# Kernel optimization log

Hardware: AMD Instinct MI355X
Metric: run time of the kernel (lower is better)

## Reference

```python
import jax, jax.numpy as jnp
import numpy as np

DIM = 1024
HEADS = 16
HEAD_DIM = DIM // HEADS  # 64
EPS = 1e-5


def layer_norm(x, w, b):
    # LayerNorm over last dim (head_dim), matching nn.LayerNorm defaults
    mu = jnp.mean(x, axis=-1, keepdims=True)
    var = jnp.mean(jnp.square(x - mu), axis=-1, keepdims=True)
    return (x - mu) * jax.lax.rsqrt(var + EPS) * w + b


def apply_rotary_emb(x, freqs):
    # x: [B, S, H, D]; freqs: [S, D/2] angles. Interleaved (complex) rotary:
    # pairs (x[2i], x[2i+1]) rotated by angle freqs[:, i].
    x1 = x[..., 0::2]
    x2 = x[..., 1::2]
    cos = jnp.cos(freqs)[None, :, None, :]
    sin = jnp.sin(freqs)[None, :, None, :]
    r1 = x1 * cos - x2 * sin
    r2 = x1 * sin + x2 * cos
    return jnp.stack([r1, r2], axis=-1).reshape(x.shape)


def setup_inputs() -> dict:
    key = jax.random.key(0)
    ks = jax.random.split(key, 8)
    B, S = 2, 2048
    x = jax.random.normal(ks[0], (B, S, DIM), dtype=jnp.float32)
    freqs = jax.random.uniform(ks[1], (S, HEAD_DIM // 2), dtype=jnp.float32)
    sc = 1.0 / np.sqrt(DIM)
    w_qkv = jax.random.normal(ks[2], (DIM, 4 * DIM), dtype=jnp.float32) * sc
    w_out = jax.random.normal(ks[3], (DIM, DIM), dtype=jnp.float32) * sc
    qn_w = jnp.ones((HEAD_DIM,), jnp.float32)
    qn_b = jnp.zeros((HEAD_DIM,), jnp.float32)
    kn_w = jnp.ones((HEAD_DIM,), jnp.float32)
    kn_b = jnp.zeros((HEAD_DIM,), jnp.float32)
    return {"x": x, "freqs": freqs, "w_qkv": w_qkv, "w_out": w_out,
            "qn_w": qn_w, "qn_b": qn_b, "kn_w": kn_w, "kn_b": kn_b}


def reference(x, freqs, w_qkv, w_out, qn_w, qn_b, kn_w, kn_b):
    B, S, _ = x.shape
    qkv = x @ w_qkv  # [B, S, 4*DIM]
    q, k, v, gate = jnp.split(qkv, 4, axis=-1)
    q = q.reshape(B, S, HEADS, HEAD_DIM)
    k = k.reshape(B, S, HEADS, HEAD_DIM)
    v = v.reshape(B, S, HEADS, HEAD_DIM)
    q = layer_norm(q, qn_w, qn_b)
    k = layer_norm(k, kn_w, kn_b)
    q = apply_rotary_emb(q, freqs)
    k = apply_rotary_emb(k, freqs)
    # flash_attn_func: non-causal softmax attention, scale 1/sqrt(head_dim)
    scale = 1.0 / np.sqrt(HEAD_DIM)
    scores = jnp.einsum('bqhd,bkhd->bhqk', q, k) * scale
    probs = jax.nn.softmax(scores, axis=-1)
    o = jnp.einsum('bhqk,bkhd->bqhd', probs, v)
    o = o.reshape(B, S, DIM)
    o = o * jax.nn.sigmoid(gate)
    return o @ w_out
```

## Files before the change

kernel.cpp:

```cpp
#include <hip/hip_runtime.h>


typedef _Float16 f16;
typedef _Float16 f16x8 __attribute__((ext_vector_type(8)));
typedef _Float16 f16x4 __attribute__((ext_vector_type(4)));
typedef float    f32x4 __attribute__((ext_vector_type(4)));

#define MFMA16(a, b, c) __builtin_amdgcn_mfma_f32_16x16x32_f16((a), (b), (c), 0, 0, 0)

__device__ __forceinline__ void gload16(const void* g, void* l) {
  __builtin_amdgcn_global_load_lds(
      (const __attribute__((address_space(1))) void*)g,
      (__attribute__((address_space(3))) void*)l, 16, 0, 0);
}

__device__ __forceinline__ float exp2_fast(float x) {
#if __has_builtin(__builtin_amdgcn_exp2f)
  return __builtin_amdgcn_exp2f(x);
#else
  float r;
  asm("v_exp_f32 %0, %1" : "=v"(r) : "v"(x));
  return r;
#endif
}
__device__ __forceinline__ unsigned pkrtz(float a, float b) {
  typedef __fp16 hf16x2 __attribute__((ext_vector_type(2)));
  union { hf16x2 h; unsigned u; } c;
  c.h = __builtin_amdgcn_cvt_pkrtz(a, b);
  return c.u;
}

__global__ void rope_table_kernel(const float* __restrict__ freqs, float* __restrict__ tbl) {
  int i = blockIdx.x * 256 + threadIdx.x;
  if (i >= 2048 * 32) return;
  int s = i >> 5, j = i & 31;
  float f = freqs[i];
  tbl[s * 64 + j]      = cosf(f);
  tbl[s * 64 + 32 + j] = sinf(f);
}

__global__ void cast_f16_kernel(const float* __restrict__ in, f16* __restrict__ out, int n8) {
  int i = blockIdx.x * 256 + threadIdx.x;
  if (i >= n8) return;
  float4 a = ((const float4*)in)[2 * i];
  float4 b = ((const float4*)in)[2 * i + 1];
  f16x8 o;
  o[0] = (f16)a.x; o[1] = (f16)a.y; o[2] = (f16)a.z; o[3] = (f16)a.w;
  o[4] = (f16)b.x; o[5] = (f16)b.y; o[6] = (f16)b.z; o[7] = (f16)b.w;
  ((f16x8*)out)[i] = o;
}

__global__ void transpose_cast_kernel(const float* __restrict__ in, f16* __restrict__ out,
                                      int R, int C) {
  __shared__ float t[64][65];
  int c0 = blockIdx.x * 64, r0 = blockIdx.y * 64;
  int tx = threadIdx.x & 15, ty = threadIdx.x >> 4;
#pragma unroll
  for (int i = 0; i < 4; ++i) {
    float4 v = *(const float4*)&in[(size_t)(r0 + ty + 16 * i) * C + c0 + tx * 4];
    t[ty + 16 * i][tx * 4 + 0] = v.x;
    t[ty + 16 * i][tx * 4 + 1] = v.y;
    t[ty + 16 * i][tx * 4 + 2] = v.z;
    t[ty + 16 * i][tx * 4 + 3] = v.w;
  }
  __syncthreads();
#pragma unroll
  for (int i = 0; i < 4; ++i) {
    int n = c0 + ty + 16 * i;
    int k = r0 + tx * 4;
    f16x4 o;
    o[0] = (f16)t[tx * 4 + 0][ty + 16 * i];
    o[1] = (f16)t[tx * 4 + 1][ty + 16 * i];
    o[2] = (f16)t[tx * 4 + 2][ty + 16 * i];
    o[3] = (f16)t[tx * 4 + 3][ty + 16 * i];
    *(f16x4*)&out[(size_t)n * R + k] = o;
  }
}

__global__ void fill_debug_kernel(float* out, int n) {
  int i = blockIdx.x * 256 + threadIdx.x;
  if (i < n) out[i] = 12345.0f;
}

template <int EPI>
__global__ __launch_bounds__(256, 2) void gemm_f16(
    const f16* __restrict__ A, const f16* __restrict__ B,
    float* __restrict__ Cout, int M, int N, int K,
    f16* __restrict__ qraw, f16* __restrict__ kraw,
    f16* __restrict__ g16, f16* __restrict__ v_t) {
  __shared__ f16 sA[2][128 * 64], sB[2][128 * 64];
  const int tid = threadIdx.x, lane = tid & 63;
  const int wave = tid >> 6, wm = wave >> 1, wn = wave & 1;
  const int lg = lane >> 4, lr = lane & 15;
  const int n0 = blockIdx.x * 128, m0 = blockIdx.y * 128;

  auto stg = [&](int k0, int p) {
#pragma unroll
    for (int r = 0; r < 4; ++r) {
      int off = (tid + r * 256) * 16;
      int row = off >> 7;
      int col = ((off & 127) ^ ((row & 7) << 4)) >> 1;
      gload16(A + (size_t)(m0 + row) * K + k0 + col, (char*)sA[p] + off);
      gload16(B + (size_t)(n0 + row) * K + k0 + col, (char*)sB[p] + off);
    }
  };

  f32x4 acc[4][4];
#pragma unroll
  for (int m = 0; m < 4; ++m)
#pragma unroll
    for (int n = 0; n < 4; ++n) acc[m][n] = (f32x4){0.f, 0.f, 0.f, 0.f};

  stg(0, 0);
  const int NT = K >> 6;
  int cur = 0;
  for (int t = 0; t < NT; ++t, cur ^= 1) {
    __syncthreads();
    if (t + 1 < NT) stg((t + 1) << 6, cur ^ 1);
#pragma unroll
    for (int ks = 0; ks < 2; ++ks) {
      f16x8 bfr[4];
#pragma unroll
      for (int n = 0; n < 4; ++n) {
        int row = wn * 64 + n * 16 + lr;
        int boff = (row << 7) + (ks << 6) + (lg << 4);
        boff ^= (row & 7) << 4;
        bfr[n] = *(const f16x8*)((const char*)sB[cur] + boff);
      }
#pragma unroll
      for (int m = 0; m < 4; ++m) {
        int row = wm * 64 + m * 16 + lr;
        int aoff = (row << 7) + (ks << 6) + (lg << 4);
        aoff ^= (row & 7) << 4;
        f16x8 afr = *(const f16x8*)((const char*)sA[cur] + aoff);
#pragma unroll
        for (int n = 0; n < 4; ++n) acc[m][n] = MFMA16(afr, bfr[n], acc[m][n]);
      }
    }
  }

  if (EPI == 0) {
#pragma unroll
    for (int m = 0; m < 4; ++m) {
      int row = m0 + wm * 64 + m * 16 + 4 * lg;
#pragma unroll
      for (int n = 0; n < 4; ++n) {
        int col = n0 + wn * 64 + n * 16 + lr;
#pragma unroll
        for (int r = 0; r < 4; ++r) Cout[(size_t)(row + r) * N + col] = acc[m][n][r];
      }
    }
  } else {
    const int region = n0 >> 10;
    if (region == 2) {
#pragma unroll
      for (int m = 0; m < 4; ++m) {
        int row = m0 + wm * 64 + m * 16 + 4 * lg;
#pragma unroll
        for (int n = 0; n < 4; ++n) {
          int col = n0 + wn * 64 + n * 16 + lr;
          int c = col - 2048, hh = c >> 6, d = c & 63;
          int bb = row >> 11, s = row & 2047;
          f16x4 pv;
          pv[0] = (f16)acc[m][n][0];
          pv[1] = (f16)acc[m][n][1];
          pv[2] = (f16)acc[m][n][2];
          pv[3] = (f16)acc[m][n][3];
          *(f16x4*)&v_t[(size_t)((bb * 16 + hh) * 64 + d) * 2048 + s] = pv;
        }
      }
    } else if (region == 3) {
#pragma unroll
      for (int m = 0; m < 4; ++m) {
        int row = m0 + wm * 64 + m * 16 + 4 * lg;
#pragma unroll
        for (int n = 0; n < 4; ++n) {
          int col = (n0 & 1023) + wn * 64 + n * 16 + lr;
#pragma unroll
          for (int r = 0; r < 4; ++r) {
            float sg = 1.0f / (1.0f + exp2_fast(acc[m][n][r] * -1.44269504f));
            g16[(size_t)(row + r) * 1024 + col] = (f16)sg;
          }
        }
      }
    } else {
      f16* dst = region ? kraw : qraw;
#pragma unroll
      for (int m = 0; m < 4; ++m) {
        int row = m0 + wm * 64 + m * 16 + 4 * lg;
#pragma unroll
        for (int n = 0; n < 4; ++n) {
          int col = (n0 & 1023) + wn * 64 + n * 16 + lr;
#pragma unroll
          for (int r = 0; r < 4; ++r)
            dst[(size_t)(row + r) * 1024 + col] = (f16)acc[m][n][r];
        }
      }
    }
  }
}

__global__ void norm_rope16_kernel(const f16* __restrict__ qr, const f16* __restrict__ kr,
                                   const float* __restrict__ tbl,
                                   const float* __restrict__ qn_w, const float* __restrict__ qn_b,
                                   const float* __restrict__ kn_w, const float* __restrict__ kn_b,
                                   f16* __restrict__ q_h, f16* __restrict__ k_h) {
  int row = blockIdx.x;
  int s = row & 2047;
  int hh = threadIdx.x >> 4, sub = threadIdx.x & 15;
  int base = row * 1024 + hh * 64 + sub * 4;
  float c0 = tbl[s * 64 + sub * 2 + 0], c1 = tbl[s * 64 + sub * 2 + 1];
  float s0 = tbl[s * 64 + 32 + sub * 2 + 0], s1 = tbl[s * 64 + 32 + sub * 2 + 1];
#pragma unroll
  for (int which = 0; which < 2; ++which) {
    const f16* src = which ? kr : qr;
    const float* wp = which ? kn_w : qn_w;
    const float* bp = which ? kn_b : qn_b;
    f16* dst = which ? k_h : q_h;
    f16x4 xr = *(const f16x4*)&src[base];
    float x0 = (float)xr[0], x1 = (float)xr[1], x2 = (float)xr[2], x3 = (float)xr[3];
    float sum = x0 + x1 + x2 + x3;
    sum += __shfl_xor(sum, 1); sum += __shfl_xor(sum, 2);
    sum += __shfl_xor(sum, 4); sum += __shfl_xor(sum, 8);
    float mu = sum * (1.0f / 64.0f);
    float d0 = x0 - mu, d1 = x1 - mu, d2 = x2 - mu, d3 = x3 - mu;
    float sq = d0 * d0 + d1 * d1 + d2 * d2 + d3 * d3;
    sq += __shfl_xor(sq, 1); sq += __shfl_xor(sq, 2);
    sq += __shfl_xor(sq, 4); sq += __shfl_xor(sq, 8);
    float rstd = rsqrtf(sq * (1.0f / 64.0f) + 1e-5f);
    float4 w = *(const float4*)&wp[sub * 4];
    float4 bb = *(const float4*)&bp[sub * 4];
    float n0 = d0 * rstd * w.x + bb.x;
    float n1 = d1 * rstd * w.y + bb.y;
    float n2 = d2 * rstd * w.z + bb.z;
    float n3 = d3 * rstd * w.w + bb.w;
    float r0 = n0 * c0 - n1 * s0, r1 = n0 * s0 + n1 * c0;
    float r2 = n2 * c1 - n3 * s1, r3 = n2 * s1 + n3 * c1;
    f16x4 ov;
    ov[0] = (f16)r0; ov[1] = (f16)r1; ov[2] = (f16)r2; ov[3] = (f16)r3;
    *(f16x4*)&dst[base] = ov;
  }
}

__global__ __launch_bounds__(256, 2) void attn_kernel(const f16* __restrict__ q_h,
                                                      const f16* __restrict__ k_h,
                                                      const f16* __restrict__ v_t,
                                                      const f16* __restrict__ g16,
                                                      f16* __restrict__ a16) {
  __shared__ __align__(16) char smem[65536];
  const int tid = threadIdx.x, lane = tid & 63, wave = tid >> 6;
  const int lg = lane >> 4, lr = lane & 15;
  const int bh = blockIdx.x >> 4, qt = blockIdx.x & 15;
  const int b = bh >> 4, h = bh & 15;
  const int qrow0 = b * 2048 + qt * 128 + wave * 32;

  auto stage = [&](int kv0, int p) {
    char* kb = smem + p * 16384;
    char* vb = smem + 32768 + p * 16384;
#pragma unroll
    for (int r = 0; r < 4; ++r) {
      int off = (tid + r * 256) * 16;
      {
        int row = off >> 7;
        int col = ((off & 127) ^ ((row & 7) << 4)) >> 1;
        int g = ((row >> 5) << 5) + (((row >> 2) & 3) << 3) + (((row >> 4) & 1) << 2) + (row & 3);
        gload16(&k_h[(size_t)(b * 2048 + kv0 + g) * 1024 + h * 64 + col], kb + off);
      }
      {
        int d = off >> 8;
        int col = ((off & 255) ^ ((d & 15) << 4)) >> 1;
        gload16(&v_t[(size_t)(bh * 64 + d) * 2048 + kv0 + col], vb + off);
      }
    }
  };

  f16x8 qf[2][2];
#pragma unroll
  for (int n = 0; n < 2; ++n)
#pragma unroll
    for (int ks = 0; ks < 2; ++ks)
      qf[n][ks] = *(const f16x8*)&q_h[(size_t)(qrow0 + n * 16 + lr) * 1024 + h * 64 + ks * 32 + lg * 8];

  f16x8 ones;
#pragma unroll
  for (int j = 0; j < 8; ++j) ones[j] = (f16)1.0f;

  f32x4 accO[4][2];
#pragma unroll
  for (int m = 0; m < 4; ++m) {
    accO[m][0] = (f32x4){0.f, 0.f, 0.f, 0.f};
    accO[m][1] = (f32x4){0.f, 0.f, 0.f, 0.f};
  }
  f32x4 accL[2] = {(f32x4){0.f, 0.f, 0.f, 0.f}, (f32x4){0.f, 0.f, 0.f, 0.f}};
  float mrun[2] = {-1e30f, -1e30f};
  const float SCL2 = 0.125f * 1.44269504f;
  const float THRP = 44.36f;
  const f32x4 fz = (f32x4){0.f, 0.f, 0.f, 0.f};

  stage(0, 0);

  int cur = 0;
  for (int t = 0; t < 16; ++t, cur ^= 1) {
    __syncthreads();
    if (t < 15) stage((t + 1) * 128, cur ^ 1);

    const char* kb = smem + cur * 16384;
    const char* vb = smem + 32768 + cur * 16384;

    f32x4 st[8][2];
    __builtin_amdgcn_s_setprio(1);
#pragma unroll
    for (int m = 0; m < 8; ++m) {
      int row = m * 16 + lr;
      int koff0 = ((row << 7) + (lg << 4)) ^ ((row & 7) << 4);
      int koff1 = ((row << 7) + 64 + (lg << 4)) ^ ((row & 7) << 4);
      f16x8 a0 = *(const f16x8*)(kb + koff0);
      f16x8 a1 = *(const f16x8*)(kb + koff1);
      st[m][0] = MFMA16(a1, qf[0][1], MFMA16(a0, qf[0][0], fz));
      st[m][1] = MFMA16(a1, qf[1][1], MFMA16(a0, qf[1][0], fz));
    }
    __builtin_amdgcn_s_setprio(0);

    uint2 pdw[2][8];
#pragma unroll
    for (int n = 0; n < 2; ++n) {
      float t03 = fmaxf(fmaxf(fmaxf(st[0][n][0], st[0][n][1]), fmaxf(st[0][n][2], st[0][n][3])),
                        fmaxf(fmaxf(st[1][n][0], st[1][n][1]), fmaxf(st[1][n][2], st[1][n][3])));
      float t47 = fmaxf(fmaxf(fmaxf(st[2][n][0], st[2][n][1]), fmaxf(st[2][n][2], st[2][n][3])),
                        fmaxf(fmaxf(st[3][n][0], st[3][n][1]), fmaxf(st[3][n][2], st[3][n][3])));
      float t8b = fmaxf(fmaxf(fmaxf(st[4][n][0], st[4][n][1]), fmaxf(st[4][n][2], st[4][n][3])),
                        fmaxf(fmaxf(st[5][n][0], st[5][n][1]), fmaxf(st[5][n][2], st[5][n][3])));
      float tcf = fmaxf(fmaxf(fmaxf(st[6][n][0], st[6][n][1]), fmaxf(st[6][n][2], st[6][n][3])),
                        fmaxf(fmaxf(st[7][n][0], st[7][n][1]), fmaxf(st[7][n][2], st[7][n][3])));
      float vm = fmaxf(fmaxf(t03, t47), fmaxf(t8b, tcf));
      vm = fmaxf(vm, __shfl_xor(vm, 16));
      vm = fmaxf(vm, __shfl_xor(vm, 32));
      if (__any(vm > mrun[n] + THRP)) {
        float mnew = fmaxf(mrun[n], vm);
        float fac = exp2_fast((mrun[n] - mnew) * SCL2);
        mrun[n] = mnew;
        accL[n] *= fac;
#pragma unroll
        for (int m = 0; m < 4; ++m) accO[m][n] *= fac;
      }
      float mc = mrun[n] * SCL2;
#pragma unroll
      for (int m = 0; m < 8; ++m) {
        float p0 = exp2_fast(st[m][n][0] * SCL2 - mc);
        float p1 = exp2_fast(st[m][n][1] * SCL2 - mc);
        float p2 = exp2_fast(st[m][n][2] * SCL2 - mc);
        float p3 = exp2_fast(st[m][n][3] * SCL2 - mc);
        pdw[n][m].x = pkrtz(p0, p1);
        pdw[n][m].y = pkrtz(p2, p3);
      }
    }

    f16x8 pb[2][4];
#pragma unroll
    for (int n = 0; n < 2; ++n)
#pragma unroll
      for (int ks = 0; ks < 4; ++ks) {
        union { uint4 u; f16x8 h; } c;
        c.u = make_uint4(pdw[n][2 * ks].x, pdw[n][2 * ks].y,
                         pdw[n][2 * ks + 1].x, pdw[n][2 * ks + 1].y);
        pb[n][ks] = c.h;
      }
    __builtin_amdgcn_s_setprio(1);
#pragma unroll
    for (int m = 0; m < 4; ++m)
#pragma unroll
      for (int ks = 0; ks < 4; ++ks) {
        int d = m * 16 + lr;
        int voff = (d << 8) + (ks << 6) + (lg << 4);
        voff ^= (d & 15) << 4;
        f16x8 av = *(const f16x8*)(vb + voff);
        accO[m][0] = MFMA16(av, pb[0][ks], accO[m][0]);
        accO[m][1] = MFMA16(av, pb[1][ks], accO[m][1]);
      }
#pragma unroll
    for (int ks = 0; ks < 4; ++ks) {
      accL[0] = MFMA16(ones, pb[0][ks], accL[0]);
      accL[1] = MFMA16(ones, pb[1][ks], accL[1]);
    }
    __builtin_amdgcn_s_setprio(0);
  }

#pragma unroll
  for (int n = 0; n < 2; ++n) {
    float rl = 1.0f / accL[n][0];
    int orow = qrow0 + n * 16 + lr;
#pragma unroll
    for (int m = 0; m < 4; ++m) {
      size_t idx = (size_t)orow * 1024 + h * 64 + m * 16 + lg * 4;
      f16x4 gv = *(const f16x4*)&g16[idx];
      f16x4 ov;
      ov[0] = (f16)(accO[m][n][0] * rl * (float)gv[0]);
      ov[1] = (f16)(accO[m][n][1] * rl * (float)gv[1]);
      ov[2] = (f16)(accO[m][n][2] * rl * (float)gv[2]);
      ov[3] = (f16)(accO[m][n][3] * rl * (float)gv[3]);
      *(f16x4*)&a16[idx] = ov;
    }
  }
}

extern "C" void kernel_launch(void* const* d_in, const int* in_sizes, int n_in,
                              void* d_out, int out_size, void* d_ws, size_t ws_size,
                              hipStream_t stream) {
  const float* x      = (const float*)d_in[0];
  const float* freqs  = (const float*)d_in[1];
  const float* w_qkv  = (const float*)d_in[2];
  const float* w_out  = (const float*)d_in[3];
  const float* qn_w   = (const float*)d_in[4];
  const float* qn_b   = (const float*)d_in[5];
  const float* kn_w   = (const float*)d_in[6];
  const float* kn_b   = (const float*)d_in[7];
  float* out = (float*)d_out;
  char* ws = (char*)d_ws;
  const size_t MB = 1024 * 1024;
  f16*   v_t   = (f16*)(ws + 0);
  f16*   x16   = (f16*)(ws + 8 * MB);
  f16*   wq16  = (f16*)(ws + 16 * MB);
  f16*   wo16  = (f16*)(ws + 24 * MB);
  f16*   qraw  = (f16*)(ws + 26 * MB);
  f16*   kraw  = (f16*)(ws + 34 * MB);
  f16*   q_h   = (f16*)(ws + 42 * MB);
  f16*   k_h   = (f16*)(ws + 50 * MB);
  f16*   g16   = (f16*)(ws + 58 * MB);
  float* tbl   = (float*)(ws + 66 * MB);
  f16*   a16   = x16;

  if (ws_size < (size_t)67 * MB) {
    fill_debug_kernel<<<(out_size + 255) / 256, 256, 0, stream>>>(out, out_size);
    return;
  }

  rope_table_kernel<<<256, 256, 0, stream>>>(freqs, tbl);
  cast_f16_kernel<<<2048, 256, 0, stream>>>(x, x16, 524288);
  transpose_cast_kernel<<<dim3(64, 16), 256, 0, stream>>>(w_qkv, wq16, 1024, 4096);
  transpose_cast_kernel<<<dim3(16, 16), 256, 0, stream>>>(w_out, wo16, 1024, 1024);

  gemm_f16<1><<<dim3(32, 32), 256, 0, stream>>>(x16, wq16, nullptr, 4096, 4096, 1024,
                                                qraw, kraw, g16, v_t);
  norm_rope16_kernel<<<4096, 256, 0, stream>>>(qraw, kraw, tbl, qn_w, qn_b, kn_w, kn_b, q_h, k_h);
  attn_kernel<<<512, 256, 0, stream>>>(q_h, k_h, v_t, g16, a16);
  gemm_f16<0><<<dim3(8, 32), 256, 0, stream>>>(a16, wo16, out, 4096, 1024, 1024,
                                               nullptr, nullptr, nullptr, nullptr);
}
```

Baseline: 150.4 us.

## Use a 256x256 tile with 512 threads for the QKV projection GEMM

Splits the templated GEMM into a dedicated QKV kernel and an output-projection kernel. The QKV kernel grows the block tile from 128x128 to 256x256, with 8 waves each computing a 128x64 sub-tile and double-buffered LDS using 128KB. It launches 256 blocks at one per CU, which raises operand reuse per byte loaded from LDS and global memory. The trade-off is lower occupancy for latency hiding and a single-wave grid, so the whole GEMM waits on its slowest block.

After: 143.9 us. -4.3%, faster.

```diff
diff --git a/kernel.cpp b/kernel.cpp
--- a/kernel.cpp
+++ b/kernel.cpp
@@ -82,12 +82,113 @@
   if (i < n) out[i] = 12345.0f;
 }
 
-template <int EPI>
-__global__ __launch_bounds__(256, 2) void gemm_f16(
-    const f16* __restrict__ A, const f16* __restrict__ B,
-    float* __restrict__ Cout, int M, int N, int K,
+__global__ __launch_bounds__(512, 1) void gemm_qkv_256(
+    const f16* __restrict__ A, const f16* __restrict__ B, int K,
     f16* __restrict__ qraw, f16* __restrict__ kraw,
     f16* __restrict__ g16, f16* __restrict__ v_t) {
+  __shared__ f16 sA[2][256 * 64], sB[2][256 * 64];
+  const int tid = threadIdx.x, lane = tid & 63;
+  const int wave = tid >> 6;
+  const int wm = wave >> 2, wn = wave & 3;
+  const int lg = lane >> 4, lr = lane & 15;
+  const int n0 = blockIdx.x * 256, m0 = blockIdx.y * 256;
+
+  auto stg = [&](int k0, int p) {
+#pragma unroll
+    for (int r = 0; r < 4; ++r) {
+      int off = (tid + r * 512) * 16;
+      int row = off >> 7;
+      int col = ((off & 127) ^ ((row & 7) << 4)) >> 1;
+      gload16(A + (size_t)(m0 + row) * K + k0 + col, (char*)sA[p] + off);
+      gload16(B + (size_t)(n0 + row) * K + k0 + col, (char*)sB[p] + off);
+    }
+  };
+
+  f32x4 acc[8][4];
+#pragma unroll
+  for (int m = 0; m < 8; ++m)
+#pragma unroll
+    for (int n = 0; n < 4; ++n) acc[m][n] = (f32x4){0.f, 0.f, 0.f, 0.f};
+
+  stg(0, 0);
+  const int NT = K >> 6;
+  int cur = 0;
+  for (int t = 0; t < NT; ++t, cur ^= 1) {
+    __syncthreads();
+    if (t + 1 < NT) stg((t + 1) << 6, cur ^ 1);
+#pragma unroll
+    for (int ks = 0; ks < 2; ++ks) {
+      f16x8 bfr[4];
+#pragma unroll
+      for (int n = 0; n < 4; ++n) {
+        int row = wn * 64 + n * 16 + lr;
+        int boff = (row << 7) + (ks << 6) + (lg << 4);
+        boff ^= (row & 7) << 4;
+        bfr[n] = *(const f16x8*)((const char*)sB[cur] + boff);
+      }
+#pragma unroll
+      for (int m = 0; m < 8; ++m) {
+        int row = wm * 128 + m * 16 + lr;
+        int aoff = (row << 7) + (ks << 6) + (lg << 4);
+        aoff ^= (row & 7) << 4;
+        f16x8 afr = *(const f16x8*)((const char*)sA[cur] + aoff);
+#pragma unroll
+        for (int n = 0; n < 4; ++n) acc[m][n] = MFMA16(afr, bfr[n], acc[m][n]);
+      }
+    }
+  }
+
+  const int region = n0 >> 10;
+  if (region == 2) {
+#pragma unroll
+    for (int m = 0; m < 8; ++m) {
+      int row = m0 + wm * 128 + m * 16 + 4 * lg;
+#pragma unroll
+      for (int n = 0; n < 4; ++n) {
+        int c = (n0 & 1023) + wn * 64 + n * 16 + lr;
+        int hh = c >> 6, d = c & 63;
+        int bb = row >> 11, s = row & 2047;
+        f16x4 pv;
+        pv[0] = (f16)acc[m][n][0];
+        pv[1] = (f16)acc[m][n][1];
+        pv[2] = (f16)acc[m][n][2];
+        pv[3] = (f16)acc[m][n][3];
+        *(f16x4*)&v_t[(size_t)((bb * 16 + hh) * 64 + d) * 2048 + s] = pv;
+      }
+    }
+  } else if (region == 3) {
+#pragma unroll
+    for (int m = 0; m < 8; ++m) {
+      int row = m0 + wm * 128 + m * 16 + 4 * lg;
+#pragma unroll
+      for (int n = 0; n < 4; ++n) {
+        int col = (n0 & 1023) + wn * 64 + n * 16 + lr;
+#pragma unroll
+        for (int r = 0; r < 4; ++r) {
+          float sg = 1.0f / (1.0f + exp2_fast(acc[m][n][r] * -1.44269504f));
+          g16[(size_t)(row + r) * 1024 + col] = (f16)sg;
+        }
+      }
+    }
+  } else {
+    f16* dst = region ? kraw : qraw;
+#pragma unroll
+    for (int m = 0; m < 8; ++m) {
+      int row = m0 + wm * 128 + m * 16 + 4 * lg;
+#pragma unroll
+      for (int n = 0; n < 4; ++n) {
+        int col = (n0 & 1023) + wn * 64 + n * 16 + lr;
+#pragma unroll
+        for (int r = 0; r < 4; ++r)
+          dst[(size_t)(row + r) * 1024 + col] = (f16)acc[m][n][r];
+      }
+    }
+  }
+}
+
+__global__ __launch_bounds__(256, 2) void gemm_out_128(
+    const f16* __restrict__ A, const f16* __restrict__ B,
+    float* __restrict__ Cout, int M, int N, int K) {
   __shared__ f16 sA[2][128 * 64], sB[2][128 * 64];
   const int tid = threadIdx.x, lane = tid & 63;
   const int wave = tid >> 6, wm = wave >> 1, wn = wave & 1;
@@ -139,63 +240,14 @@
     }
   }
 
-  if (EPI == 0) {
-#pragma unroll
-    for (int m = 0; m < 4; ++m) {
-      int row = m0 + wm * 64 + m * 16 + 4 * lg;
-#pragma unroll
-      for (int n = 0; n < 4; ++n) {
-        int col = n0 + wn * 64 + n * 16 + lr;
-#pragma unroll
-        for (int r = 0; r < 4; ++r) Cout[(size_t)(row + r) * N + col] = acc[m][n][r];
-      }
-    }
-  } else {
-    const int region = n0 >> 10;
-    if (region == 2) {
-#pragma unroll
-      for (int m = 0; m < 4; ++m) {
-        int row = m0 + wm * 64 + m * 16 + 4 * lg;
-#pragma unroll
-        for (int n = 0; n < 4; ++n) {
-          int col = n0 + wn * 64 + n * 16 + lr;
-          int c = col - 2048, hh = c >> 6, d = c & 63;
-          int bb = row >> 11, s = row & 2047;
-          f16x4 pv;
-          pv[0] = (f16)acc[m][n][0];
-          pv[1] = (f16)acc[m][n][1];
-          pv[2] = (f16)acc[m][n][2];
-          pv[3] = (f16)acc[m][n][3];
-          *(f16x4*)&v_t[(size_t)((bb * 16 + hh) * 64 + d) * 2048 + s] = pv;
-        }
-      }
-    } else if (region == 3) {
-#pragma unroll
-      for (int m = 0; m < 4; ++m) {
-        int row = m0 + wm * 64 + m * 16 + 4 * lg;
-#pragma unroll
-        for (int n = 0; n < 4; ++n) {
-          int col = (n0 & 1023) + wn * 64 + n * 16 + lr;
-#pragma unroll
-          for (int r = 0; r < 4; ++r) {
-            float sg = 1.0f / (1.0f + exp2_fast(acc[m][n][r] * -1.44269504f));
-            g16[(size_t)(row + r) * 1024 + col] = (f16)sg;
-          }
-        }
-      }
-    } else {
-      f16* dst = region ? kraw : qraw;
-#pragma unroll
-      for (int m = 0; m < 4; ++m) {
-        int row = m0 + wm * 64 + m * 16 + 4 * lg;
-#pragma unroll
-        for (int n = 0; n < 4; ++n) {
-          int col = (n0 & 1023) + wn * 64 + n * 16 + lr;
-#pragma unroll
-          for (int r = 0; r < 4; ++r)
-            dst[(size_t)(row + r) * 1024 + col] = (f16)acc[m][n][r];
-        }
-      }
+#pragma unroll
+  for (int m = 0; m < 4; ++m) {
+    int row = m0 + wm * 64 + m * 16 + 4 * lg;
+#pragma unroll
+    for (int n = 0; n < 4; ++n) {
+      int col = n0 + wn * 64 + n * 16 + lr;
+#pragma unroll
+      for (int r = 0; r < 4; ++r) Cout[(size_t)(row + r) * N + col] = acc[m][n][r];
     }
   }
 }
@@ -439,10 +491,8 @@
   transpose_cast_kernel<<<dim3(64, 16), 256, 0, stream>>>(w_qkv, wq16, 1024, 4096);
   transpose_cast_kernel<<<dim3(16, 16), 256, 0, stream>>>(w_out, wo16, 1024, 1024);
 
-  gemm_f16<1><<<dim3(32, 32), 256, 0, stream>>>(x16, wq16, nullptr, 4096, 4096, 1024,
-                                                qraw, kraw, g16, v_t);
+  gemm_qkv_256<<<dim3(16, 16), 512, 0, stream>>>(x16, wq16, 1024, qraw, kraw, g16, v_t);
   norm_rope16_kernel<<<4096, 256, 0, stream>>>(qraw, kraw, tbl, qn_w, qn_b, kn_w, kn_b, q_h, k_h);
   attn_kernel<<<512, 256, 0, stream>>>(q_h, k_h, v_t, g16, a16);
-  gemm_f16<0><<<dim3(8, 32), 256, 0, stream>>>(a16, wo16, out, 4096, 1024, 1024,
-                                               nullptr, nullptr, nullptr, nullptr);
-}
+  gemm_out_128<<<dim3(8, 32), 256, 0, stream>>>(a16, wo16, out, 4096, 1024, 1024);
+}
```
